# Optimization experiments

Hardware: AMD Instinct MI355X
Metric: run time of the kernel (lower is better)

The kernel has to match this reference:

```python
import jax, jax.numpy as jnp
import numpy as np

P = 4; PSIZE = 16; EPS = 1e-8; LAM = 1e-3; MF = 2.0; ITERS = 2
BATCH = 64; A = 64; B = 8; C = 16; D = 16; E = 10


def _conv2d(x, w, b, stride, pad):
    y = jax.lax.conv_general_dilated(x, w, (stride, stride), [(pad, pad), (pad, pad)],
                                     dimension_numbers=('NCHW', 'OIHW', 'NCHW'))
    return y + b[None, :, None, None]


def _patches(x, K, stride):
    # x: (b, H, W, F) -> (b, oh, ow, K, K, F) sliding KxK windows with given stride
    b, H, W, F = x.shape
    oh = (H - K) // stride + 1
    ow = (W - K) // stride + 1
    ih = jnp.arange(oh) * stride
    iw = jnp.arange(ow) * stride
    p = x[:, ih[:, None] + jnp.arange(K)[None, :]]          # (b, oh, K, W, F)
    p = p[:, :, :, iw[:, None] + jnp.arange(K)[None, :]]    # (b, oh, K, ow, K, F)
    return p.transpose(0, 1, 3, 2, 4, 5), oh, ow


def _fuzzy_routing(v, a_in, beta_u, beta_a):
    # Fuzzy (c-means style) routing. v: (n, N, Cout, PSIZE) votes, a_in: (n, N).
    n, N, Cc, _ = v.shape
    r = jnp.full((n, N, Cc), 1.0 / Cc, dtype=v.dtype)
    aw = a_in[:, :, None]
    for t in range(ITERS):
        rm = (r ** MF) * aw                                             # fuzzified, activation-weighted
        coeff = rm / (jnp.sum(rm, axis=1, keepdims=True) + EPS)         # (n, N, C)
        mu = jnp.einsum('bnc,bncp->bcp', coeff, v)                      # (n, C, PSIZE)
        if t < ITERS - 1:
            dist = jnp.sum((v - mu[:, None]) ** 2, axis=-1) + EPS       # (n, N, C)
            inv = dist ** (-1.0 / (MF - 1.0))
            r = inv / (jnp.sum(inv, axis=2, keepdims=True) + EPS)
    sigma_sq = jnp.einsum('bnc,bncp->bcp', coeff, (v - mu[:, None]) ** 2) + EPS
    r_sum = jnp.sum((r ** MF) * aw, axis=1)                             # (n, C)
    cost = (beta_u[None, :, None] + 0.5 * jnp.log(sigma_sq)) * r_sum[:, :, None]
    a_out = jax.nn.sigmoid(LAM * (beta_a[None, :] - jnp.sum(cost, axis=2)))
    return mu, a_out


def _conv_caps(pose, a, W, beta_u, beta_a, K, stride):
    # pose: (b, H, W, Bi, PSIZE), a: (b, H, W, Bi); W: (K*K*Bi, Co, P, P)
    b, H, Wd, Bi, _ = pose.shape
    Co = W.shape[1]
    pp, oh, ow = _patches(pose.reshape(b, H, Wd, Bi * PSIZE), K, stride)
    ap, _, _ = _patches(a, K, stride)
    n = b * oh * ow
    pp = pp.reshape(n, K * K * Bi, P, P)
    ap = ap.reshape(n, K * K * Bi)
    v = jnp.einsum('nipq,icqr->nicpr', pp, W).reshape(n, K * K * Bi, Co, PSIZE)
    mu, a_out = _fuzzy_routing(v, ap, beta_u, beta_a)
    return mu.reshape(b, oh, ow, Co, PSIZE), a_out.reshape(b, oh, ow, Co)


def _class_caps(pose, a, W, beta_u, beta_a):
    # K=1, weight-shared over positions, with coordinate addition.
    b, H, Wd, Bi, _ = pose.shape
    Co = W.shape[1]
    v = jnp.einsum('bhwipq,icqr->bhwicpr', pose.reshape(b, H, Wd, Bi, P, P), W)
    v = v.reshape(b, H, Wd, Bi, Co, PSIZE)
    ch = (jnp.arange(H, dtype=v.dtype) / H)[None, :, None, None, None]
    cw = (jnp.arange(Wd, dtype=v.dtype) / Wd)[None, None, :, None, None]
    v = v.at[..., 0].add(ch)
    v = v.at[..., 1].add(cw)
    v = v.reshape(b, H * Wd * Bi, Co, PSIZE)
    return _fuzzy_routing(v, a.reshape(b, -1), beta_u, beta_a)


def setup_inputs():
    key = jax.random.key(0)
    ks = jax.random.split(key, 8)
    return {
        'x': jax.random.normal(ks[0], (BATCH, 1, 32, 32), jnp.float32),
        'conv1_w': jax.random.normal(ks[1], (A, 1, 5, 5), jnp.float32) * 0.1,
        'conv1_b': jnp.zeros((A,), jnp.float32),
        'bn_g': jnp.ones((A,), jnp.float32),
        'bn_b': jnp.zeros((A,), jnp.float32),
        'bn_mean': jnp.zeros((A,), jnp.float32),
        'bn_var': jnp.ones((A,), jnp.float32),
        'prim_pose_w': jax.random.normal(ks[2], (B * PSIZE, A, 1, 1), jnp.float32) * 0.1,
        'prim_pose_b': jnp.zeros((B * PSIZE,), jnp.float32),
        'prim_a_w': jax.random.normal(ks[3], (B, A, 1, 1), jnp.float32) * 0.1,
        'prim_a_b': jnp.zeros((B,), jnp.float32),
        'w1': jax.random.normal(ks[4], (3 * 3 * B, C, P, P), jnp.float32),
        'bu1': jnp.zeros((C,), jnp.float32),
        'ba1': jnp.zeros((C,), jnp.float32),
        'w2': jax.random.normal(ks[5], (3 * 3 * C, D, P, P), jnp.float32),
        'bu2': jnp.zeros((D,), jnp.float32),
        'ba2': jnp.zeros((D,), jnp.float32),
        'wc': jax.random.normal(ks[6], (D, E, P, P), jnp.float32),
        'buc': jnp.zeros((E,), jnp.float32),
        'bac': jnp.zeros((E,), jnp.float32),
    }


def reference(x, conv1_w, conv1_b, bn_g, bn_b, bn_mean, bn_var,
              prim_pose_w, prim_pose_b, prim_a_w, prim_a_b,
              w1, bu1, ba1, w2, bu2, ba2, wc, buc, bac):
    y = _conv2d(x, conv1_w, conv1_b, 2, 2)                               # (b, A, 16, 16)
    inv_std = jax.lax.rsqrt(bn_var + 1e-3)
    y = (y - bn_mean[None, :, None, None]) * (bn_g * inv_std)[None, :, None, None] + bn_b[None, :, None, None]
    y = jax.nn.relu(y)
    pose = _conv2d(y, prim_pose_w, prim_pose_b, 1, 0)                    # (b, B*16, 16, 16)
    a = jax.nn.sigmoid(_conv2d(y, prim_a_w, prim_a_b, 1, 0))             # (b, B, 16, 16)
    b_, _, H, Wd = a.shape
    pose = pose.transpose(0, 2, 3, 1).reshape(b_, H, Wd, B, PSIZE)
    a = a.transpose(0, 2, 3, 1)
    pose1, a1 = _conv_caps(pose, a, w1, bu1, ba1, 3, 2)
    pose2, a2 = _conv_caps(pose1, a1, w2, bu2, ba2, 3, 1)
    _, a_class = _class_caps(pose2, a2, wc, buc, bac)                    # (b, E)
    return a_class
```

## Files before the change

### kernel.cpp

```cpp
#include <hip/hip_runtime.h>
#include <math.h>

#define EPS_ 1e-8f
#define LAM_ 1e-3f

__global__ __launch_bounds__(256) void k_conv_bn(
    const float* __restrict__ x, const float* __restrict__ cw, const float* __restrict__ cb,
    const float* __restrict__ g, const float* __restrict__ bb,
    const float* __restrict__ mean, const float* __restrict__ var,
    float* __restrict__ y)
{
    int t = blockIdx.x * 256 + threadIdx.x;
    int ch = t & 63, w = (t >> 6) & 15, h = (t >> 10) & 15, b = t >> 14;
    const float* xb = x + b * 1024;
    const float* wc = cw + ch * 25;
    float acc = cb[ch];
    #pragma unroll
    for (int kh = 0; kh < 5; ++kh) {
        int ih = h * 2 - 2 + kh;
        if (ih < 0 || ih > 31) continue;
        #pragma unroll
        for (int kw = 0; kw < 5; ++kw) {
            int iw = w * 2 - 2 + kw;
            if (iw < 0 || iw > 31) continue;
            acc = fmaf(xb[ih * 32 + iw], wc[kh * 5 + kw], acc);
        }
    }
    float v = (acc - mean[ch]) * (g[ch] * rsqrtf(var[ch] + 1e-3f)) + bb[ch];
    y[t] = fmaxf(v, 0.f);
}

__global__ __launch_bounds__(256) void k_transw(
    const float* __restrict__ w1, const float* __restrict__ w2, const float* __restrict__ wc,
    const float* __restrict__ pw, const float* __restrict__ pb,
    const float* __restrict__ aw, const float* __restrict__ ab,
    float* __restrict__ w1t, float* __restrict__ w2t, float* __restrict__ wct,
    float* __restrict__ wpt)
{
    int t = blockIdx.x * 256 + threadIdx.x;
    if (t < 3616 * 16) {
        int m = t >> 4, e = t & 15, r = e >> 2, q = e & 3;
        const float* src; float* dst;
        if (m < 1152)      { src = w1 + m * 16;          dst = w1t + m * 16; }
        else if (m < 3456) { src = w2 + (m - 1152) * 16; dst = w2t + (m - 1152) * 16; }
        else               { src = wc + (m - 3456) * 16; dst = wct + (m - 3456) * 16; }
        dst[e] = src[q * 4 + r];
    } else if (t < 3616 * 16 + 65 * 136) {
        int idx = t - 3616 * 16;
        int o = idx % 136, j = idx / 136;
        float v;
        if (j == 64)       v = (o < 128) ? pb[o] : ab[o - 128];
        else if (o < 128)  v = pw[o * 64 + j];
        else               v = aw[(o - 128) * 64 + j];
        wpt[j * 136 + o] = v;
    }
}

__global__ __launch_bounds__(256) void k_prim(
    const float* __restrict__ y, const float* __restrict__ wpt,
    float* __restrict__ poseP, float* __restrict__ aP)
{
    int t = blockIdx.x * 256 + threadIdx.x;
    if (t >= 16384 * 34) return;
    int oq = t % 34;
    int pos = t / 34;
    const float* yp = y + pos * 64;
    float4 acc = *(const float4*)(wpt + 64 * 136 + oq * 4);
    #pragma unroll
    for (int j0 = 0; j0 < 64; j0 += 4) {
        float4 y4 = *(const float4*)(yp + j0);
        float4 w0 = *(const float4*)(wpt + (j0 + 0) * 136 + oq * 4);
        float4 w1 = *(const float4*)(wpt + (j0 + 1) * 136 + oq * 4);
        float4 w2 = *(const float4*)(wpt + (j0 + 2) * 136 + oq * 4);
        float4 w3 = *(const float4*)(wpt + (j0 + 3) * 136 + oq * 4);
        acc.x = fmaf(y4.x, w0.x, fmaf(y4.y, w1.x, fmaf(y4.z, w2.x, fmaf(y4.w, w3.x, acc.x))));
        acc.y = fmaf(y4.x, w0.y, fmaf(y4.y, w1.y, fmaf(y4.z, w2.y, fmaf(y4.w, w3.y, acc.y))));
        acc.z = fmaf(y4.x, w0.z, fmaf(y4.y, w1.z, fmaf(y4.z, w2.z, fmaf(y4.w, w3.z, acc.z))));
        acc.w = fmaf(y4.x, w0.w, fmaf(y4.y, w1.w, fmaf(y4.z, w2.w, fmaf(y4.w, w3.w, acc.w))));
    }
    if (oq < 32) {
        ((float4*)(poseP + pos * 128))[oq] = acc;
    } else {
        int oo = (oq - 32) * 4;
        float* ad = aP + pos * 8 + oo;
        ad[0] = 1.f / (1.f + __expf(-acc.x));
        ad[1] = 1.f / (1.f + __expf(-acc.y));
        ad[2] = 1.f / (1.f + __expf(-acc.z));
        ad[3] = 1.f / (1.f + __expf(-acc.w));
    }
}

template<int N, int C, int K, int S, int H, int W, int Bi, int OH, int OW>
__global__ __launch_bounds__(128) void k_caps_wave(
    const float* __restrict__ pose_in,
    const float* __restrict__ a_in,
    const float* __restrict__ Wt,
    const float* __restrict__ bu, const float* __restrict__ ba,
    float* __restrict__ pose_out,
    float* __restrict__ a_out)
{
    static_assert(C == 16 && N % 4 == 0, "");
    constexpr int NIT = N / 4;

    __shared__ __align__(16) float pp[2 * N * 16];
    __shared__ float ap[2 * N];

    const int t = threadIdx.x;
    const int w = t >> 6, lane = t & 63;
    float* ppw = pp + w * N * 16;
    float* apw = ap + w * N;

    const int n_ = blockIdx.x * 2 + w;
    const int b = n_ / (OH * OW);
    const int rem = n_ % (OH * OW);
    const int oh = rem / OW, ow = rem % OW;

    for (int idx = lane; idx < N * 4; idx += 64) {
        int i = idx >> 2, f = idx & 3;
        int bi = i % Bi;
        int k2 = i / Bi;
        int sw = ow * S + (k2 % K), sh = oh * S + (k2 / K);
        const float4* src = (const float4*)(pose_in + (((b * H + sh) * W + sw) * Bi + bi) * 16);
        ((float4*)(ppw + i * 16))[f] = src[f];
    }
    for (int i = lane; i < N; i += 64) {
        int bi = i % Bi;
        int k2 = i / Bi;
        int sw = ow * S + (k2 % K), sh = oh * S + (k2 / K);
        apw[i] = a_in[((b * H + sh) * W + sw) * Bi + bi];
    }
    __syncthreads();

    float suma = 0.f;
    for (int i = lane; i < N; i += 64) suma += apw[i];
    #pragma unroll
    for (int m = 1; m < 64; m <<= 1) suma += __shfl_xor(suma, m, 64);
    const float inv0 = __builtin_amdgcn_rcpf(suma + (float)(C * C) * EPS_);

    const int ig = t >> 4 & 3, cc = t & 15;

    float muU[16];
    #pragma unroll
    for (int e2 = 0; e2 < 16; ++e2) muU[e2] = 0.f;
    #pragma unroll 2
    for (int ii = 0; ii < NIT; ++ii) {
        int i = ig + ii * 4;
        const float4* pi4 = (const float4*)(ppw + i * 16);
        const float4* wt4 = (const float4*)(Wt + (i * C + cc) * 16);
        float4 pv[4] = { pi4[0], pi4[1], pi4[2], pi4[3] };
        float4 wv[4] = { wt4[0], wt4[1], wt4[2], wt4[3] };
        float co = apw[i] * inv0;
        #pragma unroll
        for (int e2 = 0; e2 < 16; ++e2) {
            float4 p4 = pv[e2 >> 2], w4 = wv[e2 & 3];
            float v = p4.x * w4.x + p4.y * w4.y + p4.z * w4.z + p4.w * w4.w;
            muU[e2] = fmaf(co, v, muU[e2]);
        }
    }
    #pragma unroll
    for (int e2 = 0; e2 < 16; ++e2) {
        muU[e2] += __shfl_xor(muU[e2], 16, 64);
        muU[e2] += __shfl_xor(muU[e2], 32, 64);
    }

    float SvU[16], Sv2U[16];
    #pragma unroll
    for (int e2 = 0; e2 < 16; ++e2) { SvU[e2] = 0.f; Sv2U[e2] = 0.f; }
    float rsum = 0.f;
    #pragma unroll 2
    for (int ii = 0; ii < NIT; ++ii) {
        int i = ig + ii * 4;
        const float4* pi4 = (const float4*)(ppw + i * 16);
        const float4* wt4 = (const float4*)(Wt + (i * C + cc) * 16);
        float4 pv[4] = { pi4[0], pi4[1], pi4[2], pi4[3] };
        float4 wv[4] = { wt4[0], wt4[1], wt4[2], wt4[3] };
        float vv[16];
        float dist = EPS_;
        #pragma unroll
        for (int e2 = 0; e2 < 16; ++e2) {
            float4 p4 = pv[e2 >> 2], w4 = wv[e2 & 3];
            float v = p4.x * w4.x + p4.y * w4.y + p4.z * w4.z + p4.w * w4.w;
            vv[e2] = v;
            float d = v - muU[e2];
            dist = fmaf(d, d, dist);
        }
        float inv = __builtin_amdgcn_rcpf(dist);
        float s = inv;
        #pragma unroll
        for (int m = 1; m < 16; m <<= 1) s += __shfl_xor(s, m, 64);
        float r1 = inv * __builtin_amdgcn_rcpf(s + EPS_);
        float rm = r1 * r1 * apw[i];
        rsum += rm;
        #pragma unroll
        for (int e2 = 0; e2 < 16; ++e2) {
            float rv = rm * vv[e2];
            SvU[e2] += rv;
            Sv2U[e2] = fmaf(rv, vv[e2], Sv2U[e2]);
        }
    }
    #pragma unroll
    for (int e2 = 0; e2 < 16; ++e2) {
        SvU[e2] += __shfl_xor(SvU[e2], 16, 64);
        SvU[e2] += __shfl_xor(SvU[e2], 32, 64);
        Sv2U[e2] += __shfl_xor(Sv2U[e2], 16, 64);
        Sv2U[e2] += __shfl_xor(Sv2U[e2], 32, 64);
    }
    rsum += __shfl_xor(rsum, 16, 64);
    rsum += __shfl_xor(rsum, 32, 64);

    const float id = 1.f / (rsum + EPS_);
    const float S0 = rsum * id;
    const float buc_ = bu[cc];
    float cs = 0.f;
    float4 outv[4];
    #pragma unroll
    for (int e2 = 0; e2 < 16; ++e2) {
        float Sv = SvU[e2] * id;
        float Sv2 = Sv2U[e2] * id;
        float sigma = fmaxf(Sv2 + Sv * Sv * (S0 - 2.f), 0.f) + EPS_;
        cs += (buc_ + 0.5f * __logf(sigma)) * rsum;
        ((float*)outv)[e2] = Sv;
    }
    if (lane < 16) {
        float4* pd = (float4*)(pose_out + (n_ * C + cc) * 16);
        pd[0] = outv[0]; pd[1] = outv[1]; pd[2] = outv[2]; pd[3] = outv[3];
        a_out[n_ * C + cc] = 1.f / (1.f + __expf(-(LAM_ * (ba[cc] - cs))));
    }
}

template<int N, int C, int H, int W, int Bi, int BLK>
__global__ __launch_bounds__(BLK) void k_caps_class(
    const float* __restrict__ pose_in, const float* __restrict__ a_in,
    const float* __restrict__ Wt,
    const float* __restrict__ bu, const float* __restrict__ ba,
    float* __restrict__ a_out)
{
    constexpr int NW  = BLK / 64;
    constexpr int NIG = BLK / 16;
    constexpr int NIT = (N + NIG - 1) / NIG;

    __shared__ __align__(16) float pp[N * 16];
    __shared__ float ap[N];
    __shared__ float coeff0[N];
    __shared__ float mu0[16 * 17];
    __shared__ float red1[NW * C * 17];
    __shared__ float red2[NW * C * 17];
    __shared__ float redr[NW * C];

    const int t = threadIdx.x;
    const int lane = t & 63;
    const int w = t >> 6;
    const int b = blockIdx.x;

    for (int idx = t; idx < N * 4; idx += BLK) {
        int i = idx >> 2, f = idx & 3;
        int bi = i % Bi;
        int hw = i / Bi;
        int sw = hw % W, sh = hw / W;
        const float4* src = (const float4*)(pose_in + (((b * H + sh) * W + sw) * Bi + bi) * 16);
        ((float4*)(pp + i * 16))[f] = src[f];
    }
    for (int i = t; i < N; i += BLK) {
        int bi = i % Bi;
        int hw = i / Bi;
        int sw = hw % W, sh = hw / W;
        ap[i] = a_in[((b * H + sh) * W + sw) * Bi + bi];
    }
    __syncthreads();

    {
        float part = 0.f;
        for (int i = t; i < N; i += BLK) part += ap[i];
        #pragma unroll
        for (int m = 1; m < 64; m <<= 1) part += __shfl_xor(part, m, 64);
        if (lane == 0) red1[w] = part;
        __syncthreads();
        float s = 0.f;
        #pragma unroll
        for (int ww = 0; ww < NW; ++ww) s += red1[ww];
        float inv0 = 1.f / (s + (float)(C * C) * EPS_);
        for (int i = t; i < N; i += BLK) coeff0[i] = ap[i] * inv0;
        __syncthreads();
    }

    const int ig = t >> 4, cc = t & 15;

    {
        float muU[16];
        #pragma unroll
        for (int e2 = 0; e2 < 16; ++e2) muU[e2] = 0.f;
        if (cc < C) {
            for (int ii = 0; ii < NIT; ++ii) {
                int i = ig + ii * NIG;
                if (i < N) {
                    const float4* pi4 = (const float4*)(pp + i * 16);
                    const float4* wt4 = (const float4*)(Wt + ((i % Bi) * C + cc) * 16);
                    float4 pv[4] = { pi4[0], pi4[1], pi4[2], pi4[3] };
                    float4 wv[4] = { wt4[0], wt4[1], wt4[2], wt4[3] };
                    float co = coeff0[i];
                    float chv = (float)(i / (W * Bi)) * (1.f / H);
                    float cwv = (float)((i / Bi) % W) * (1.f / W);
                    #pragma unroll
                    for (int e2 = 0; e2 < 16; ++e2) {
                        float4 p4 = pv[e2 >> 2], w4 = wv[e2 & 3];
                        float v = p4.x * w4.x + p4.y * w4.y + p4.z * w4.z + p4.w * w4.w;
                        if (e2 == 0) v += chv;
                        if (e2 == 1) v += cwv;
                        muU[e2] = fmaf(co, v, muU[e2]);
                    }
                }
            }
        }
        #pragma unroll
        for (int e2 = 0; e2 < 16; ++e2) {
            float xv = muU[e2];
            xv += __shfl_xor(xv, 16, 64);
            xv += __shfl_xor(xv, 32, 64);
            if (lane < 16 && lane < C) red1[(w * C + lane) * 17 + e2] = xv;
        }
        __syncthreads();
        if (t < 256) {
            int c = t >> 4, e = t & 15;
            if (c < C) {
                float m = 0.f;
                #pragma unroll
                for (int ww = 0; ww < NW; ++ww) m += red1[(ww * C + c) * 17 + e];
                mu0[c * 17 + e] = m;
            }
        }
        __syncthreads();
    }

    {
        float m0[16];
        if (cc < C) {
            #pragma unroll
            for (int e2 = 0; e2 < 16; ++e2) m0[e2] = mu0[cc * 17 + e2];
        }
        float SvU[16], Sv2U[16];
        #pragma unroll
        for (int e2 = 0; e2 < 16; ++e2) { SvU[e2] = 0.f; Sv2U[e2] = 0.f; }
        float rsumP = 0.f;

        for (int ii = 0; ii < NIT; ++ii) {
            int i = ig + ii * NIG;
            bool act = (i < N);
            float inv = 0.f;
            float vv[16];
            if (act && cc < C) {
                const float4* pi4 = (const float4*)(pp + i * 16);
                const float4* wt4 = (const float4*)(Wt + ((i % Bi) * C + cc) * 16);
                float4 pv[4] = { pi4[0], pi4[1], pi4[2], pi4[3] };
                float4 wv[4] = { wt4[0], wt4[1], wt4[2], wt4[3] };
                float chv = (float)(i / (W * Bi)) * (1.f / H);
                float cwv = (float)((i / Bi) % W) * (1.f / W);
                float dist = EPS_;
                #pragma unroll
                for (int e2 = 0; e2 < 16; ++e2) {
                    float4 p4 = pv[e2 >> 2], w4 = wv[e2 & 3];
                    float v = p4.x * w4.x + p4.y * w4.y + p4.z * w4.z + p4.w * w4.w;
                    if (e2 == 0) v += chv;
                    if (e2 == 1) v += cwv;
                    vv[e2] = v;
                    float d = v - m0[e2];
                    dist = fmaf(d, d, dist);
                }
                inv = 1.f / dist;
            }
            float s = inv;
            #pragma unroll
            for (int m = 1; m < 16; m <<= 1) s += __shfl_xor(s, m, 64);
            if (act && cc < C) {
                float r1 = inv / (s + EPS_);
                float rm = r1 * r1 * ap[i];
                rsumP += rm;
                #pragma unroll
                for (int e2 = 0; e2 < 16; ++e2) {
                    SvU[e2] = fmaf(rm, vv[e2], SvU[e2]);
                    Sv2U[e2] = fmaf(rm * vv[e2], vv[e2], Sv2U[e2]);
                }
            }
        }
        #pragma unroll
        for (int e2 = 0; e2 < 16; ++e2) {
            float xv = SvU[e2];
            xv += __shfl_xor(xv, 16, 64);
            xv += __shfl_xor(xv, 32, 64);
            float yv = Sv2U[e2];
            yv += __shfl_xor(yv, 16, 64);
            yv += __shfl_xor(yv, 32, 64);
            if (lane < 16 && lane < C) {
                red1[(w * C + lane) * 17 + e2] = xv;
                red2[(w * C + lane) * 17 + e2] = yv;
            }
        }
        {
            float rv = rsumP;
            rv += __shfl_xor(rv, 16, 64);
            rv += __shfl_xor(rv, 32, 64);
            if (lane < 16 && lane < C) redr[w * C + lane] = rv;
        }
        __syncthreads();
    }

    if (t < 256) {
        int c = t >> 4, e = t & 15;
        if (c < C) {
            float SvT = 0.f, Sv2T = 0.f, R = 0.f;
            #pragma unroll
            for (int ww = 0; ww < NW; ++ww) {
                SvT  += red1[(ww * C + c) * 17 + e];
                Sv2T += red2[(ww * C + c) * 17 + e];
                R    += redr[ww * C + c];
            }
            float id = 1.f / (R + EPS_);
            float S0 = R * id;
            float Sv = SvT * id;
            float Sv2 = Sv2T * id;
            float sigma = fmaxf(Sv2 + Sv * Sv * (S0 - 2.f), 0.f) + EPS_;
            float cost = (bu[c] + 0.5f * logf(sigma)) * R;
            float cs = cost;
            #pragma unroll
            for (int m = 1; m < 16; m <<= 1) cs += __shfl_xor(cs, m, 64);
            if (e == 0) a_out[b * C + c] = 1.f / (1.f + expf(-(LAM_ * (ba[c] - cs))));
        }
    }
}

extern "C" void kernel_launch(void* const* d_in, const int* in_sizes, int n_in,
                              void* d_out, int out_size, void* d_ws, size_t ws_size,
                              hipStream_t stream)
{
    const float* x   = (const float*)d_in[0];
    const float* c1w = (const float*)d_in[1];
    const float* c1b = (const float*)d_in[2];
    const float* bng = (const float*)d_in[3];
    const float* bnb = (const float*)d_in[4];
    const float* bnm = (const float*)d_in[5];
    const float* bnv = (const float*)d_in[6];
    const float* ppw = (const float*)d_in[7];
    const float* ppb = (const float*)d_in[8];
    const float* paw = (const float*)d_in[9];
    const float* pab = (const float*)d_in[10];
    const float* w1  = (const float*)d_in[11];
    const float* bu1 = (const float*)d_in[12];
    const float* ba1 = (const float*)d_in[13];
    const float* w2  = (const float*)d_in[14];
    const float* bu2 = (const float*)d_in[15];
    const float* ba2 = (const float*)d_in[16];
    const float* wcp = (const float*)d_in[17];
    const float* buc = (const float*)d_in[18];
    const float* bac = (const float*)d_in[19];
    float* out = (float*)d_out;

    float* ws    = (float*)d_ws;
    float* y     = ws;
    float* poseP = y + 1048576;
    float* aP    = poseP + 2097152;
    float* pose1 = aP + 131072;
    float* a1    = pose1 + 802816;
    float* pose2 = a1 + 50176;
    float* a2    = pose2 + 409600;
    float* w1t   = a2 + 25600;
    float* w2t   = w1t + 18432;
    float* wct   = w2t + 36864;
    float* wpt   = wct + 2560;

    hipLaunchKernelGGL(k_transw, dim3((3616 * 16 + 65 * 136 + 255) / 256), dim3(256), 0, stream,
                       w1, w2, wcp, ppw, ppb, paw, pab, w1t, w2t, wct, wpt);
    hipLaunchKernelGGL(k_conv_bn, dim3(4096), dim3(256), 0, stream,
                       x, c1w, c1b, bng, bnb, bnm, bnv, y);
    hipLaunchKernelGGL(k_prim, dim3((16384 * 34 + 255) / 256), dim3(256), 0, stream,
                       y, wpt, poseP, aP);
    hipLaunchKernelGGL((k_caps_wave<72, 16, 3, 2, 16, 16, 8, 7, 7>), dim3(1568), dim3(128), 0, stream,
                       poseP, aP, w1t, bu1, ba1, pose1, a1);
    hipLaunchKernelGGL((k_caps_wave<144, 16, 3, 1, 7, 7, 16, 5, 5>), dim3(800), dim3(128), 0, stream,
                       pose1, a1, w2t, bu2, ba2, pose2, a2);
    hipLaunchKernelGGL((k_caps_class<400, 10, 5, 5, 16, 1024>), dim3(64), dim3(1024), 0, stream,
                       pose2, a2, wct, buc, bac, out);
}
```

Before: 253.8 us.

## Fuse conv and weight transpose, use single-wave caps blocks, fast math intrinsics

Measured after the change: 259.9 us. 2.4% more time.

```diff
diff --git a/kernel.cpp b/kernel.cpp
--- a/kernel.cpp
+++ b/kernel.cpp
@@ -4,55 +4,54 @@
 #define EPS_ 1e-8f
 #define LAM_ 1e-3f
 
-__global__ __launch_bounds__(256) void k_conv_bn(
+__global__ __launch_bounds__(256) void k_conv_transw(
     const float* __restrict__ x, const float* __restrict__ cw, const float* __restrict__ cb,
     const float* __restrict__ g, const float* __restrict__ bb,
     const float* __restrict__ mean, const float* __restrict__ var,
-    float* __restrict__ y)
-{
-    int t = blockIdx.x * 256 + threadIdx.x;
-    int ch = t & 63, w = (t >> 6) & 15, h = (t >> 10) & 15, b = t >> 14;
-    const float* xb = x + b * 1024;
-    const float* wc = cw + ch * 25;
-    float acc = cb[ch];
-    #pragma unroll
-    for (int kh = 0; kh < 5; ++kh) {
-        int ih = h * 2 - 2 + kh;
-        if (ih < 0 || ih > 31) continue;
-        #pragma unroll
-        for (int kw = 0; kw < 5; ++kw) {
-            int iw = w * 2 - 2 + kw;
-            if (iw < 0 || iw > 31) continue;
-            acc = fmaf(xb[ih * 32 + iw], wc[kh * 5 + kw], acc);
-        }
-    }
-    float v = (acc - mean[ch]) * (g[ch] * rsqrtf(var[ch] + 1e-3f)) + bb[ch];
-    y[t] = fmaxf(v, 0.f);
-}
-
-__global__ __launch_bounds__(256) void k_transw(
+    float* __restrict__ y,
     const float* __restrict__ w1, const float* __restrict__ w2, const float* __restrict__ wc,
     const float* __restrict__ pw, const float* __restrict__ pb,
     const float* __restrict__ aw, const float* __restrict__ ab,
     float* __restrict__ w1t, float* __restrict__ w2t, float* __restrict__ wct,
     float* __restrict__ wpt)
 {
-    int t = blockIdx.x * 256 + threadIdx.x;
-    if (t < 3616 * 16) {
-        int m = t >> 4, e = t & 15, r = e >> 2, q = e & 3;
-        const float* src; float* dst;
-        if (m < 1152)      { src = w1 + m * 16;          dst = w1t + m * 16; }
-        else if (m < 3456) { src = w2 + (m - 1152) * 16; dst = w2t + (m - 1152) * 16; }
-        else               { src = wc + (m - 3456) * 16; dst = wct + (m - 3456) * 16; }
-        dst[e] = src[q * 4 + r];
-    } else if (t < 3616 * 16 + 65 * 136) {
-        int idx = t - 3616 * 16;
-        int o = idx % 136, j = idx / 136;
-        float v;
-        if (j == 64)       v = (o < 128) ? pb[o] : ab[o - 128];
-        else if (o < 128)  v = pw[o * 64 + j];
-        else               v = aw[(o - 128) * 64 + j];
-        wpt[j * 136 + o] = v;
+    if (blockIdx.x < 4096) {
+        int t = blockIdx.x * 256 + threadIdx.x;
+        int ch = t & 63, w = (t >> 6) & 15, h = (t >> 10) & 15, b = t >> 14;
+        const float* xb = x + b * 1024;
+        const float* wc_ = cw + ch * 25;
+        float acc = cb[ch];
+        #pragma unroll
+        for (int kh = 0; kh < 5; ++kh) {
+            int ih = h * 2 - 2 + kh;
+            if (ih < 0 || ih > 31) continue;
+            #pragma unroll
+            for (int kw = 0; kw < 5; ++kw) {
+                int iw = w * 2 - 2 + kw;
+                if (iw < 0 || iw > 31) continue;
+                acc = fmaf(xb[ih * 32 + iw], wc_[kh * 5 + kw], acc);
+            }
+        }
+        float v = (acc - mean[ch]) * (g[ch] * rsqrtf(var[ch] + 1e-3f)) + bb[ch];
+        y[t] = fmaxf(v, 0.f);
+    } else {
+        int t = (blockIdx.x - 4096) * 256 + threadIdx.x;
+        if (t < 3616 * 16) {
+            int m = t >> 4, e = t & 15, r = e >> 2, q = e & 3;
+            const float* src; float* dst;
+            if (m < 1152)      { src = w1 + m * 16;          dst = w1t + m * 16; }
+            else if (m < 3456) { src = w2 + (m - 1152) * 16; dst = w2t + (m - 1152) * 16; }
+            else               { src = wc + (m - 3456) * 16; dst = wct + (m - 3456) * 16; }
+            dst[e] = src[q * 4 + r];
+        } else if (t < 3616 * 16 + 65 * 136) {
+            int idx = t - 3616 * 16;
+            int o = idx % 136, j = idx / 136;
+            float v;
+            if (j == 64)       v = (o < 128) ? pb[o] : ab[o - 128];
+            else if (o < 128)  v = pw[o * 64 + j];
+            else               v = aw[(o - 128) * 64 + j];
+            wpt[j * 136 + o] = v;
+        }
     }
 }
 
@@ -91,7 +90,7 @@
 }
 
 template<int N, int C, int K, int S, int H, int W, int Bi, int OH, int OW>
-__global__ __launch_bounds__(128) void k_caps_wave(
+__global__ __launch_bounds__(64) void k_caps_w1(
     const float* __restrict__ pose_in,
     const float* __restrict__ a_in,
     const float* __restrict__ Wt,
@@ -99,111 +98,120 @@
     float* __restrict__ pose_out,
     float* __restrict__ a_out)
 {
-    static_assert(C == 16 && N % 4 == 0, "");
+    static_assert(C == 16 && N % 8 == 0, "");
     constexpr int NIT = N / 4;
-
-    __shared__ __align__(16) float pp[2 * N * 16];
-    __shared__ float ap[2 * N];
-
-    const int t = threadIdx.x;
-    const int w = t >> 6, lane = t & 63;
-    float* ppw = pp + w * N * 16;
-    float* apw = ap + w * N;
-
-    const int n_ = blockIdx.x * 2 + w;
+    constexpr int NP  = NIT / 2;
+
+    __shared__ __align__(16) float pp[N * 16];
+    __shared__ float ap[N];
+
+    const int lane = threadIdx.x;
+    const int n_ = blockIdx.x;
     const int b = n_ / (OH * OW);
     const int rem = n_ % (OH * OW);
     const int oh = rem / OW, ow = rem % OW;
 
     for (int idx = lane; idx < N * 4; idx += 64) {
         int i = idx >> 2, f = idx & 3;
-        int bi = i % Bi;
-        int k2 = i / Bi;
+        int bi = i % Bi, k2 = i / Bi;
         int sw = ow * S + (k2 % K), sh = oh * S + (k2 / K);
-        const float4* src = (const float4*)(pose_in + (((b * H + sh) * W + sw) * Bi + bi) * 16);
-        ((float4*)(ppw + i * 16))[f] = src[f];
+        ((float4*)(pp + i * 16))[f] =
+            ((const float4*)(pose_in + (((b * H + sh) * W + sw) * Bi + bi) * 16))[f];
     }
     for (int i = lane; i < N; i += 64) {
-        int bi = i % Bi;
-        int k2 = i / Bi;
+        int bi = i % Bi, k2 = i / Bi;
         int sw = ow * S + (k2 % K), sh = oh * S + (k2 / K);
-        apw[i] = a_in[((b * H + sh) * W + sw) * Bi + bi];
+        ap[i] = a_in[((b * H + sh) * W + sw) * Bi + bi];
     }
     __syncthreads();
 
     float suma = 0.f;
-    for (int i = lane; i < N; i += 64) suma += apw[i];
+    for (int i = lane; i < N; i += 64) suma += ap[i];
     #pragma unroll
     for (int m = 1; m < 64; m <<= 1) suma += __shfl_xor(suma, m, 64);
     const float inv0 = __builtin_amdgcn_rcpf(suma + (float)(C * C) * EPS_);
 
-    const int ig = t >> 4 & 3, cc = t & 15;
-
-    float muU[16];
-    #pragma unroll
-    for (int e2 = 0; e2 < 16; ++e2) muU[e2] = 0.f;
-    #pragma unroll 2
+    const int ig = (lane >> 4) & 3, cc = lane & 15;
+
+    float mu[16];
+    #pragma unroll
+    for (int e2 = 0; e2 < 16; ++e2) mu[e2] = 0.f;
     for (int ii = 0; ii < NIT; ++ii) {
         int i = ig + ii * 4;
-        const float4* pi4 = (const float4*)(ppw + i * 16);
+        const float4* pi4 = (const float4*)(pp + i * 16);
         const float4* wt4 = (const float4*)(Wt + (i * C + cc) * 16);
         float4 pv[4] = { pi4[0], pi4[1], pi4[2], pi4[3] };
         float4 wv[4] = { wt4[0], wt4[1], wt4[2], wt4[3] };
-        float co = apw[i] * inv0;
+        float co = ap[i] * inv0;
         #pragma unroll
         for (int e2 = 0; e2 < 16; ++e2) {
             float4 p4 = pv[e2 >> 2], w4 = wv[e2 & 3];
             float v = p4.x * w4.x + p4.y * w4.y + p4.z * w4.z + p4.w * w4.w;
-            muU[e2] = fmaf(co, v, muU[e2]);
+            mu[e2] = fmaf(co, v, mu[e2]);
         }
     }
     #pragma unroll
     for (int e2 = 0; e2 < 16; ++e2) {
-        muU[e2] += __shfl_xor(muU[e2], 16, 64);
-        muU[e2] += __shfl_xor(muU[e2], 32, 64);
-    }
-
-    float SvU[16], Sv2U[16];
-    #pragma unroll
-    for (int e2 = 0; e2 < 16; ++e2) { SvU[e2] = 0.f; Sv2U[e2] = 0.f; }
+        mu[e2] += __shfl_xor(mu[e2], 16, 64);
+        mu[e2] += __shfl_xor(mu[e2], 32, 64);
+    }
+
+    float Sv[16], Sv2[16];
+    #pragma unroll
+    for (int e2 = 0; e2 < 16; ++e2) { Sv[e2] = 0.f; Sv2[e2] = 0.f; }
     float rsum = 0.f;
-    #pragma unroll 2
-    for (int ii = 0; ii < NIT; ++ii) {
-        int i = ig + ii * 4;
-        const float4* pi4 = (const float4*)(ppw + i * 16);
-        const float4* wt4 = (const float4*)(Wt + (i * C + cc) * 16);
-        float4 pv[4] = { pi4[0], pi4[1], pi4[2], pi4[3] };
-        float4 wv[4] = { wt4[0], wt4[1], wt4[2], wt4[3] };
-        float vv[16];
-        float dist = EPS_;
+    for (int jj = 0; jj < NP; ++jj) {
+        int i0 = ig + (2 * jj) * 4;
+        int i1 = i0 + 4;
+        const float4* p04 = (const float4*)(pp + i0 * 16);
+        const float4* w04 = (const float4*)(Wt + (i0 * C + cc) * 16);
+        const float4* p14 = (const float4*)(pp + i1 * 16);
+        const float4* w14 = (const float4*)(Wt + (i1 * C + cc) * 16);
+        float4 pv0[4] = { p04[0], p04[1], p04[2], p04[3] };
+        float4 wv0[4] = { w04[0], w04[1], w04[2], w04[3] };
+        float4 pv1[4] = { p14[0], p14[1], p14[2], p14[3] };
+        float4 wv1[4] = { w14[0], w14[1], w14[2], w14[3] };
+        float vv0[16], vv1[16];
+        float d0 = EPS_, d1 = EPS_;
         #pragma unroll
         for (int e2 = 0; e2 < 16; ++e2) {
-            float4 p4 = pv[e2 >> 2], w4 = wv[e2 & 3];
-            float v = p4.x * w4.x + p4.y * w4.y + p4.z * w4.z + p4.w * w4.w;
-            vv[e2] = v;
-            float d = v - muU[e2];
-            dist = fmaf(d, d, dist);
-        }
-        float inv = __builtin_amdgcn_rcpf(dist);
-        float s = inv;
-        #pragma unroll
-        for (int m = 1; m < 16; m <<= 1) s += __shfl_xor(s, m, 64);
-        float r1 = inv * __builtin_amdgcn_rcpf(s + EPS_);
-        float rm = r1 * r1 * apw[i];
-        rsum += rm;
+            float4 a4 = pv0[e2 >> 2], x4 = wv0[e2 & 3];
+            float4 b4 = pv1[e2 >> 2], y4 = wv1[e2 & 3];
+            float v0 = a4.x * x4.x + a4.y * x4.y + a4.z * x4.z + a4.w * x4.w;
+            float v1 = b4.x * y4.x + b4.y * y4.y + b4.z * y4.z + b4.w * y4.w;
+            vv0[e2] = v0; vv1[e2] = v1;
+            float e0 = v0 - mu[e2];
+            float e1 = v1 - mu[e2];
+            d0 = fmaf(e0, e0, d0);
+            d1 = fmaf(e1, e1, d1);
+        }
+        float inv_0 = __builtin_amdgcn_rcpf(d0);
+        float inv_1 = __builtin_amdgcn_rcpf(d1);
+        float s0 = inv_0, s1 = inv_1;
+        #pragma unroll
+        for (int m = 1; m < 16; m <<= 1) {
+            s0 += __shfl_xor(s0, m, 64);
+            s1 += __shfl_xor(s1, m, 64);
+        }
+        float r10 = inv_0 * __builtin_amdgcn_rcpf(s0 + EPS_);
+        float r11 = inv_1 * __builtin_amdgcn_rcpf(s1 + EPS_);
+        float rm0 = r10 * r10 * ap[i0];
+        float rm1 = r11 * r11 * ap[i1];
+        rsum += rm0 + rm1;
         #pragma unroll
         for (int e2 = 0; e2 < 16; ++e2) {
-            float rv = rm * vv[e2];
-            SvU[e2] += rv;
-            Sv2U[e2] = fmaf(rv, vv[e2], Sv2U[e2]);
+            float rv0 = rm0 * vv0[e2];
+            float rv1 = rm1 * vv1[e2];
+            Sv[e2] += rv0 + rv1;
+            Sv2[e2] = fmaf(rv0, vv0[e2], fmaf(rv1, vv1[e2], Sv2[e2]));
         }
     }
     #pragma unroll
     for (int e2 = 0; e2 < 16; ++e2) {
-        SvU[e2] += __shfl_xor(SvU[e2], 16, 64);
-        SvU[e2] += __shfl_xor(SvU[e2], 32, 64);
-        Sv2U[e2] += __shfl_xor(Sv2U[e2], 16, 64);
-        Sv2U[e2] += __shfl_xor(Sv2U[e2], 32, 64);
+        Sv[e2] += __shfl_xor(Sv[e2], 16, 64);
+        Sv[e2] += __shfl_xor(Sv[e2], 32, 64);
+        Sv2[e2] += __shfl_xor(Sv2[e2], 16, 64);
+        Sv2[e2] += __shfl_xor(Sv2[e2], 32, 64);
     }
     rsum += __shfl_xor(rsum, 16, 64);
     rsum += __shfl_xor(rsum, 32, 64);
@@ -215,11 +223,11 @@
     float4 outv[4];
     #pragma unroll
     for (int e2 = 0; e2 < 16; ++e2) {
-        float Sv = SvU[e2] * id;
-        float Sv2 = Sv2U[e2] * id;
-        float sigma = fmaxf(Sv2 + Sv * Sv * (S0 - 2.f), 0.f) + EPS_;
+        float sv = Sv[e2] * id;
+        float sv2 = Sv2[e2] * id;
+        float sigma = fmaxf(sv2 + sv * sv * (S0 - 2.f), 0.f) + EPS_;
         cs += (buc_ + 0.5f * __logf(sigma)) * rsum;
-        ((float*)outv)[e2] = Sv;
+        ((float*)outv)[e2] = sv;
     }
     if (lane < 16) {
         float4* pd = (float4*)(pose_out + (n_ * C + cc) * 16);
@@ -278,7 +286,7 @@
         float s = 0.f;
         #pragma unroll
         for (int ww = 0; ww < NW; ++ww) s += red1[ww];
-        float inv0 = 1.f / (s + (float)(C * C) * EPS_);
+        float inv0 = __builtin_amdgcn_rcpf(s + (float)(C * C) * EPS_);
         for (int i = t; i < N; i += BLK) coeff0[i] = ap[i] * inv0;
         __syncthreads();
     }
@@ -365,13 +373,13 @@
                     float d = v - m0[e2];
                     dist = fmaf(d, d, dist);
                 }
-                inv = 1.f / dist;
+                inv = __builtin_amdgcn_rcpf(dist);
             }
             float s = inv;
             #pragma unroll
             for (int m = 1; m < 16; m <<= 1) s += __shfl_xor(s, m, 64);
             if (act && cc < C) {
-                float r1 = inv / (s + EPS_);
+                float r1 = inv * __builtin_amdgcn_rcpf(s + EPS_);
                 float rm = r1 * r1 * ap[i];
                 rsumP += rm;
                 #pragma unroll
@@ -418,11 +426,11 @@
             float Sv = SvT * id;
             float Sv2 = Sv2T * id;
             float sigma = fmaxf(Sv2 + Sv * Sv * (S0 - 2.f), 0.f) + EPS_;
-            float cost = (bu[c] + 0.5f * logf(sigma)) * R;
+            float cost = (bu[c] + 0.5f * __logf(sigma)) * R;
             float cs = cost;
             #pragma unroll
             for (int m = 1; m < 16; m <<= 1) cs += __shfl_xor(cs, m, 64);
-            if (e == 0) a_out[b * C + c] = 1.f / (1.f + expf(-(LAM_ * (ba[c] - cs))));
+            if (e == 0) a_out[b * C + c] = 1.f / (1.f + __expf(-(LAM_ * (ba[c] - cs))));
         }
     }
 }
@@ -466,15 +474,15 @@
     float* wct   = w2t + 36864;
     float* wpt   = wct + 2560;
 
-    hipLaunchKernelGGL(k_transw, dim3((3616 * 16 + 65 * 136 + 255) / 256), dim3(256), 0, stream,
+    const int transw_blocks = (3616 * 16 + 65 * 136 + 255) / 256;
+    hipLaunchKernelGGL(k_conv_transw, dim3(4096 + transw_blocks), dim3(256), 0, stream,
+                       x, c1w, c1b, bng, bnb, bnm, bnv, y,
                        w1, w2, wcp, ppw, ppb, paw, pab, w1t, w2t, wct, wpt);
-    hipLaunchKernelGGL(k_conv_bn, dim3(4096), dim3(256), 0, stream,
-                       x, c1w, c1b, bng, bnb, bnm, bnv, y);
     hipLaunchKernelGGL(k_prim, dim3((16384 * 34 + 255) / 256), dim3(256), 0, stream,
                        y, wpt, poseP, aP);
-    hipLaunchKernelGGL((k_caps_wave<72, 16, 3, 2, 16, 16, 8, 7, 7>), dim3(1568), dim3(128), 0, stream,
+    hipLaunchKernelGGL((k_caps_w1<72, 16, 3, 2, 16, 16, 8, 7, 7>), dim3(3136), dim3(64), 0, stream,
                        poseP, aP, w1t, bu1, ba1, pose1, a1);
-    hipLaunchKernelGGL((k_caps_wave<144, 16, 3, 1, 7, 7, 16, 5, 5>), dim3(800), dim3(128), 0, stream,
+    hipLaunchKernelGGL((k_caps_w1<144, 16, 3, 1, 7, 7, 16, 5, 5>), dim3(1600), dim3(64), 0, stream,
                        pose1, a1, w2t, bu2, ba2, pose2, a2);
     hipLaunchKernelGGL((k_caps_class<400, 10, 5, 5, 16, 1024>), dim3(64), dim3(1024), 0, stream,
                        pose2, a2, wct, buc, bac, out);
```
